# Optimization experiments

Measured on AMD Instinct MI355X. Metric: run time of the kernel, lower is better.

The kernel has to match this reference:

```python
import jax, jax.numpy as jnp
import numpy as np

B, N, D, K, H, L = 4, 20000, 64, 256, 4, 2
F = 4 * D
DH = D // H
SCALE = DH ** -0.5
EPS = 1e-5


def _layernorm(x, g, b):
    m = jnp.mean(x, axis=-1, keepdims=True)
    v = jnp.mean(jnp.square(x - m), axis=-1, keepdims=True)
    return (x - m) / jnp.sqrt(v + EPS) * g + b


def setup_inputs() -> dict:
    key = jax.random.key(0)
    ks = jax.random.split(key, 12)
    s = 0.02
    return {
        'expr': jax.random.normal(ks[0], (B, N), jnp.float32),
        'emb': jax.random.normal(ks[1], (N, D), jnp.float32),
        'Wq': jax.random.normal(ks[2], (L, D, D), jnp.float32) * s,
        'Wk': jax.random.normal(ks[3], (L, D, D), jnp.float32) * s,
        'Wv': jax.random.normal(ks[4], (L, D, D), jnp.float32) * s,
        'projK': jax.random.normal(ks[5], (L, N, K), jnp.float32) * s,
        'projV': jax.random.normal(ks[6], (L, N, K), jnp.float32) * s,
        'Wo': jax.random.normal(ks[7], (L, D, D), jnp.float32) * s,
        'bo': jnp.zeros((L, D), jnp.float32),
        'g1': jnp.ones((L, D), jnp.float32),
        'be1': jnp.zeros((L, D), jnp.float32),
        'W1': jax.random.normal(ks[8], (L, D, F), jnp.float32) * s,
        'bf1': jnp.zeros((L, F), jnp.float32),
        'W2': jax.random.normal(ks[9], (L, F, D), jnp.float32) * s,
        'bf2': jnp.zeros((L, D), jnp.float32),
        'g2': jnp.ones((L, D), jnp.float32),
        'be2': jnp.zeros((L, D), jnp.float32),
    }


def _forward(expr, emb, Wq, Wk, Wv, projK, projV, Wo, bo, g1, be1, W1, bf1, W2, bf2, g2, be2):
    # gene_ids = arange(N) for every batch row -> embedding lookup is just the table
    x = emb[None, :, :] * expr[:, :, None]  # [B, N, D]
    for i in range(L):
        b = x.shape[0]
        # Linformer self-attention
        q = jnp.einsum('bnd,de->bne', x, Wq[i])                 # [B, N, D]
        k_low = jnp.einsum('bnd,nk->bkd', x, projK[i])          # [B, K, D]
        v_low = jnp.einsum('bnd,nk->bkd', x, projV[i])          # [B, K, D]
        k = jnp.einsum('bkd,de->bke', k_low, Wk[i])             # [B, K, D]
        v = jnp.einsum('bkd,de->bke', v_low, Wv[i])             # [B, K, D]
        qh = q.reshape(b, N, H, DH).transpose(0, 2, 1, 3)       # [B, H, N, DH]
        kh = k.reshape(b, K, H, DH).transpose(0, 2, 1, 3)       # [B, H, K, DH]
        vh = v.reshape(b, K, H, DH).transpose(0, 2, 1, 3)       # [B, H, K, DH]
        dots = jnp.einsum('bhnd,bhkd->bhnk', qh, kh) * SCALE    # [B, H, N, K]
        attn = jax.nn.softmax(dots, axis=-1)
        o = jnp.einsum('bhnk,bhkd->bhnd', attn, vh)             # [B, H, N, DH]
        o = o.transpose(0, 2, 1, 3).reshape(b, N, D)
        o = jnp.einsum('bnd,de->bne', o, Wo[i]) + bo[i]
        x = _layernorm(o + x, g1[i], be1[i])
        # FFN (exact GELU, matching torch nn.GELU default)
        h = jax.nn.gelu(jnp.einsum('bnd,df->bnf', x, W1[i]) + bf1[i], approximate=False)
        f = jnp.einsum('bnf,fd->bnd', h, W2[i]) + bf2[i]
        x = _layernorm(f + x, g2[i], be2[i])
    return x


def reference(expr, emb, Wq, Wk, Wv, projK, projV, Wo, bo, g1, be1, W1, bf1, W2, bf2, g2, be2):
    return _forward(expr, emb, Wq, Wk, Wv, projK, projV, Wo, bo, g1, be1, W1, bf1, W2, bf2, g2, be2)
```

## Files before the change

### kernel.cpp

```cpp
#include <hip/hip_runtime.h>

using u16 = unsigned short;
typedef __bf16 bf16x8 __attribute__((ext_vector_type(8)));
typedef u16    u16x8  __attribute__((ext_vector_type(8)));
typedef u16    u16x4  __attribute__((ext_vector_type(4)));
typedef float  f32x4  __attribute__((ext_vector_type(4)));
typedef float  f32x16 __attribute__((ext_vector_type(16)));
typedef unsigned uint4v __attribute__((ext_vector_type(4)));

#define DEV static __device__ __forceinline__

constexpr int NB = 4;
constexpr int NN = 20000;
constexpr int DD = 64;
constexpr int KK = 256;
constexpr int ROWS = NB * NN;

DEV float b2f(u16 u) { union { unsigned i; float f; } c; c.i = ((unsigned)u) << 16; return c.f; }
DEV u16 f2b(float f) {
  union { float f; unsigned i; } c; c.f = f;
  unsigned i = c.i + 0x7FFFu + ((c.i >> 16) & 1u);
  return (u16)(i >> 16);
}
DEV bf16x8 ldb8(const u16* p) { return *reinterpret_cast<const bf16x8*>(p); }
DEV f32x16 mfma32(bf16x8 a, bf16x8 b, f32x16 c) { return __builtin_amdgcn_mfma_f32_32x32x16_bf16(a, b, c, 0, 0, 0); }

DEV unsigned cvtpk(float lo, float hi) {
  unsigned r;
  asm("v_cvt_pk_bf16_f32 %0, %1, %2" : "=v"(r) : "v"(lo), "v"(hi));
  return r;
}
DEV void swap32(unsigned& a, unsigned& b) {
  auto r = __builtin_amdgcn_permlane32_swap((int)a, (int)b, false, false);
  a = (unsigned)r[0]; b = (unsigned)r[1];
}

__global__ __launch_bounds__(256) void k_pre(
    const float* __restrict__ expr, const float* __restrict__ emb,
    const float* __restrict__ Wq, const float* __restrict__ Wo,
    const float* __restrict__ W1, const float* __restrict__ W2,
    const float* __restrict__ projK, const float* __restrict__ projV,
    u16* __restrict__ wb, u16* __restrict__ pKT, u16* __restrict__ pVT,
    u16* __restrict__ xb, u16* __restrict__ ones) {
  int bid = blockIdx.x;
  int t = threadIdx.x;
  if (bid < 2512) {
    int nt = bid % 157, q = bid / 157, kt = q & 3, z = q >> 2;
    int layer = z & 1, pv = z >> 1;
    const float* src = (pv ? projV : projK) + (size_t)layer * NN * KK;
    u16* dst = (pv ? pVT : pKT) + (size_t)layer * KK * NN;
    int k = kt * 64 + (t & 63);
    int n0 = nt * 128 + (t >> 6) * 32;
    if (n0 >= NN) return;
    float v[32];
#pragma unroll
    for (int i = 0; i < 32; ++i) v[i] = src[(size_t)(n0 + i) * KK + k];
    unsigned ov[16];
#pragma unroll
    for (int i2 = 0; i2 < 16; ++i2) ov[i2] = cvtpk(v[2 * i2], v[2 * i2 + 1]);
    u16* drow = dst + (size_t)k * NN + n0;
#pragma unroll
    for (int p = 0; p < 4; ++p) {
      uint4v o; o.x = ov[p * 4 + 0]; o.y = ov[p * 4 + 1]; o.z = ov[p * 4 + 2]; o.w = ov[p * 4 + 3];
      *reinterpret_cast<uint4v*>(&drow[p * 8]) = o;
    }
  } else if (bid < 5012) {
    int idx8 = ((bid - 2512) * 256 + t) * 8;
    int b = idx8 / (NN * DD);
    int rem = idx8 - b * (NN * DD);
    int n = rem >> 6, d = rem & 63;
    float4 e0 = *reinterpret_cast<const float4*>(&emb[(n << 6) + d]);
    float4 e1 = *reinterpret_cast<const float4*>(&emb[(n << 6) + d + 4]);
    float s = expr[b * NN + n];
    u16x8 o;
    o[0] = f2b(e0.x * s); o[1] = f2b(e0.y * s); o[2] = f2b(e0.z * s); o[3] = f2b(e0.w * s);
    o[4] = f2b(e1.x * s); o[5] = f2b(e1.y * s); o[6] = f2b(e1.z * s); o[7] = f2b(e1.w * s);
    *reinterpret_cast<u16x8*>(&xb[idx8]) = o;
  } else if (bid < 5076) {
    int b2 = bid - 5012;
    int bx = b2 & 7, m = (b2 >> 3) & 3, l = b2 >> 5;
    int slot = bx * 256 + t;
    u16x8 o;
    if (m <= 1) {
      if (slot >= 512) return;
      int s = slot >> 7, rem = slot & 127;
      int ct = rem >> 6, lane = rem & 63;
      int hi = lane >> 5, lo = lane & 31;
      const float* src = (m == 0 ? Wq : Wo) + l * 4096;
      u16* dst = wb + (m == 0 ? 0 : 8192) + l * 4096;
#pragma unroll
      for (int j = 0; j < 8; ++j) o[j] = f2b(src[(s * 16 + hi * 8 + j) * 64 + ct * 32 + lo]);
      *reinterpret_cast<u16x8*>(&dst[slot * 8]) = o;
    } else if (m == 2) {
      int ftile = slot >> 8, s = (slot >> 6) & 3, lane = slot & 63;
      int hi = lane >> 5, lo = lane & 31;
      const float* src = W1 + l * 16384;
      u16* dst = wb + 16384 + l * 16384;
#pragma unroll
      for (int j = 0; j < 8; ++j) o[j] = f2b(src[(s * 16 + hi * 8 + j) * 256 + ftile * 32 + lo]);
      *reinterpret_cast<u16x8*>(&dst[slot * 8]) = o;
    } else {
      int dtile = slot >> 10, s2 = (slot >> 6) & 15, lane = slot & 63;
      int hi = lane >> 5, lo = lane & 31;
      const float* src = W2 + l * 16384;
      u16* dst = wb + 49152 + l * 16384;
#pragma unroll
      for (int j = 0; j < 8; ++j) o[j] = f2b(src[(s2 * 16 + hi * 8 + j) * 64 + dtile * 32 + lo]);
      *reinterpret_cast<u16x8*>(&dst[slot * 8]) = o;
    }
  } else {
    ones[t] = 0x3F80;
  }
}

__global__ __launch_bounds__(256) void k_qxt(
    const u16* __restrict__ x, const u16* __restrict__ WB,
    u16* __restrict__ qb, u16* __restrict__ xT) {
  int bid = blockIdx.x;
  int t = threadIdx.x;
  if (bid < 625) {
    int w = t >> 6, lane = t & 63;
    int lo = lane & 31, hi = lane >> 5;
    int unit = bid * 4 + w;
    bf16x8 wf[4][2];
#pragma unroll
    for (int s = 0; s < 4; ++s)
#pragma unroll
      for (int ct = 0; ct < 2; ++ct) wf[s][ct] = ldb8(&WB[((s * 2 + ct) * 64 + lane) * 8]);
    f32x16 acc[2] = {};
    int r0 = unit * 32;
#pragma unroll
    for (int s = 0; s < 4; ++s) {
      bf16x8 a = ldb8(&x[(size_t)(r0 + lo) * 64 + s * 16 + hi * 8]);
      acc[0] = mfma32(a, wf[s][0], acc[0]);
      acc[1] = mfma32(a, wf[s][1], acc[1]);
    }
#pragma unroll
    for (int reg = 0; reg < 16; ++reg) {
      int row = r0 + (reg & 3) + 8 * (reg >> 2) + 4 * hi;
      qb[(size_t)row * 64 + lo] = f2b(acc[0][reg]);
      qb[(size_t)row * 64 + 32 + lo] = f2b(acc[1][reg]);
    }
  } else {
    int v = bid - 625;
    int nt = v % 157, b = v / 157;
    int d = t & 63;
    int n0 = nt * 128 + (t >> 6) * 32;
    if (n0 >= NN) return;
    const u16* xbp = x + (size_t)b * NN * 64;
    u16 vv[32];
#pragma unroll
    for (int i = 0; i < 32; ++i) vv[i] = xbp[(size_t)(n0 + i) * 64 + d];
    u16* dst = xT + (size_t)b * 64 * NN + (size_t)d * NN + n0;
#pragma unroll
    for (int p = 0; p < 4; ++p) {
      u16x8 o;
#pragma unroll
      for (int j = 0; j < 8; ++j) o[j] = vv[p * 8 + j];
      *reinterpret_cast<u16x8*>(&dst[p * 8]) = o;
    }
  }
}

__global__ __launch_bounds__(256) void k_proj(
    const u16* __restrict__ xT, const u16* __restrict__ pKT_l, const u16* __restrict__ pVT_l,
    float* __restrict__ part) {
  int c = blockIdx.x, b = blockIdx.y, proj = blockIdx.z;
  const u16* P = proj ? pVT_l : pKT_l;
  int t = threadIdx.x, w = t >> 6, lane = t & 63;
  int lo = lane & 31, hi = lane >> 5;
  int d0 = (w & 1) * 32;
  int kbase = (w >> 1) * 128;
  int n0 = c * 512;
  int rem = NN - n0;
  int steps = (rem < 512 ? rem : 512) >> 4;
  const u16* xr = xT + ((size_t)b * 64 + d0 + lo) * NN;
  f32x16 acc[4] = {};
  int s = 0;
  for (; s + 4 <= steps; s += 4) {
    bf16x8 a[4]; bf16x8 bv[4][4];
#pragma unroll
    for (int u = 0; u < 4; ++u) {
      int nb = n0 + (s + u) * 16 + hi * 8;
      a[u] = ldb8(&xr[nb]);
#pragma unroll
      for (int g = 0; g < 4; ++g) bv[u][g] = ldb8(&P[(size_t)(kbase + g * 32 + lo) * NN + nb]);
    }
#pragma unroll
    for (int u = 0; u < 4; ++u)
#pragma unroll
      for (int g = 0; g < 4; ++g) acc[g] = mfma32(a[u], bv[u][g], acc[g]);
  }
  for (; s < steps; ++s) {
    int nb = n0 + s * 16 + hi * 8;
    bf16x8 a = ldb8(&xr[nb]);
#pragma unroll
    for (int g = 0; g < 4; ++g) acc[g] = mfma32(a, ldb8(&P[(size_t)(kbase + g * 32 + lo) * NN + nb]), acc[g]);
  }
  float* dst = part + ((size_t)(proj * NB + b) * 40 + c) * (64 * 256);
#pragma unroll
  for (int g = 0; g < 4; ++g)
#pragma unroll
    for (int r = 0; r < 16; ++r) {
      int d = d0 + (r & 3) + 8 * (r >> 2) + 4 * hi;
      dst[d * 256 + kbase + g * 32 + lo] = acc[g][r];
    }
}

__global__ __launch_bounds__(256) void k_p2(
    const float* __restrict__ part, const float* __restrict__ Wk_l, const float* __restrict__ Wv_l,
    u16* __restrict__ kbuf, u16* __restrict__ vT) {
  int ks = blockIdx.x, b = blockIdx.y, proj = blockIdx.z;
  int k0 = ks * 8;
  const float* W = proj ? Wv_l : Wk_l;
  __shared__ float low[64][8];
  int t = threadIdx.x;
  const float* src = part + (size_t)(proj * NB + b) * 40 * (64 * 256);
#pragma unroll
  for (int i = 0; i < 2; ++i) {
    int idx = i * 256 + t;
    int e = idx >> 3, k = idx & 7;
    float s = 0.f;
    for (int cc = 0; cc < 40; ++cc) s += src[(size_t)cc * (64 * 256) + e * 256 + k0 + k];
    low[e][k] = s;
  }
  __syncthreads();
#pragma unroll
  for (int i = 0; i < 2; ++i) {
    int idx = i * 256 + t;
    int d = idx & 63, kk = idx >> 6;
    float a = 0.f;
#pragma unroll
    for (int e = 0; e < 64; ++e) a += low[e][kk] * W[e * 64 + d];
    if (proj == 0) {
      kbuf[((size_t)b * KK + k0 + kk) * 64 + d] = f2b(a * 0.3606737602222409f);
    } else {
      vT[((size_t)b * 64 + d) * KK + k0 + kk] = f2b(a);
    }
  }
}

__global__ __launch_bounds__(256) void k_attn(
    const u16* __restrict__ q, const u16* __restrict__ kbuf, const u16* __restrict__ vT,
    const u16* __restrict__ ones, u16* __restrict__ ao) {
  int t = threadIdx.x, h = t >> 6, lane = t & 63;
  int lo = lane & 31, hi = lane >> 5;
  int b = blockIdx.y;
  int n0 = blockIdx.x * 32;
  const u16* qb = q + (size_t)b * NN * 64;
  const u16* kb = kbuf + (size_t)b * KK * 64 + h * 16;
  const u16* vsrc = (lo < 16)
      ? vT + (size_t)b * 64 * KK + (size_t)(h * 16 + lo) * KK
      : ones;
  bf16x8 qf = ldb8(&qb[(size_t)(n0 + lo) * 64 + h * 16 + hi * 8]);
  f32x16 acc = {};
#pragma unroll
  for (int kt = 0; kt < 8; ++kt) {
    bf16x8 kf = ldb8(&kb[(size_t)(kt * 32 + lo) * 64 + hi * 8]);
    f32x16 z = {};
    f32x16 s = mfma32(kf, qf, z);
    float e[16];
#pragma unroll
    for (int r = 0; r < 16; ++r) e[r] = __builtin_amdgcn_exp2f(s[r]);
#pragma unroll
    for (int c = 0; c < 2; ++c) {
      unsigned Aw = cvtpk(e[c * 8 + 0], e[c * 8 + 1]);
      unsigned Bw = cvtpk(e[c * 8 + 2], e[c * 8 + 3]);
      unsigned Cw = cvtpk(e[c * 8 + 4], e[c * 8 + 5]);
      unsigned Dw = cvtpk(e[c * 8 + 6], e[c * 8 + 7]);
      swap32(Aw, Cw);
      swap32(Bw, Dw);
      uint4v pk; pk.x = Aw; pk.y = Bw; pk.z = Cw; pk.w = Dw;
      bf16x8 af = ldb8(&vsrc[kt * 32 + c * 16 + hi * 8]);
      acc = mfma32(af, __builtin_bit_cast(bf16x8, pk), acc);
    }
  }
  float inv = __builtin_amdgcn_rcpf(acc[8]);
  float o[8];
#pragma unroll
  for (int r = 0; r < 8; ++r) o[r] = acc[r] * inv;
  unsigned Aw = cvtpk(o[0], o[1]);
  unsigned Bw = cvtpk(o[2], o[3]);
  unsigned Cw = cvtpk(o[4], o[5]);
  unsigned Dw = cvtpk(o[6], o[7]);
  swap32(Aw, Cw);
  swap32(Bw, Dw);
  uint4v st; st.x = Aw; st.y = Bw; st.z = Cw; st.w = Dw;
  *reinterpret_cast<uint4v*>(&ao[(size_t)b * NN * 64 + (size_t)(n0 + lo) * 64 + h * 16 + hi * 8]) = st;
}

__global__ __launch_bounds__(256) void k_oln(
    const u16* __restrict__ A, const u16* __restrict__ WB,
    const float* __restrict__ bias, const u16* __restrict__ res,
    const float* __restrict__ g, const float* __restrict__ be, u16* __restrict__ out) {
  int t = threadIdx.x, w = t >> 6, lane = t & 63;
  int lo = lane & 31, hi = lane >> 5;
  int unit = blockIdx.x * 4 + w;
  bf16x8 wf[4][2];
#pragma unroll
  for (int s = 0; s < 4; ++s)
#pragma unroll
    for (int ct = 0; ct < 2; ++ct) wf[s][ct] = ldb8(&WB[((s * 2 + ct) * 64 + lane) * 8]);
  float bia[2], gg[2], bb[2];
#pragma unroll
  for (int ct = 0; ct < 2; ++ct) {
    bia[ct] = bias[ct * 32 + lo];
    gg[ct] = g[ct * 32 + lo];
    bb[ct] = be[ct * 32 + lo];
  }
  f32x16 acc[2] = {};
  int r0 = unit * 32;
#pragma unroll
  for (int s = 0; s < 4; ++s) {
    bf16x8 a = ldb8(&A[(size_t)(r0 + lo) * 64 + s * 16 + hi * 8]);
    acc[0] = mfma32(a, wf[s][0], acc[0]);
    acc[1] = mfma32(a, wf[s][1], acc[1]);
  }
#pragma unroll
  for (int reg = 0; reg < 16; ++reg) {
    int row = r0 + (reg & 3) + 8 * (reg >> 2) + 4 * hi;
    float a0 = acc[0][reg] + bia[0] + b2f(res[(size_t)row * 64 + lo]);
    float a1 = acc[1][reg] + bia[1] + b2f(res[(size_t)row * 64 + 32 + lo]);
    float su = a0 + a1, sq = a0 * a0 + a1 * a1;
#pragma unroll
    for (int m = 1; m <= 16; m <<= 1) { su += __shfl_xor(su, m); sq += __shfl_xor(sq, m); }
    float mean = su * (1.f / 64.f);
    float var = sq * (1.f / 64.f) - mean * mean;
    float rstd = rsqrtf(var + 1e-5f);
    out[(size_t)row * 64 + lo] = f2b((a0 - mean) * rstd * gg[0] + bb[0]);
    out[(size_t)row * 64 + 32 + lo] = f2b((a1 - mean) * rstd * gg[1] + bb[1]);
  }
}

__global__ __launch_bounds__(256) void k_ffn(
    const u16* __restrict__ A, const u16* __restrict__ W1T, const u16* __restrict__ W2T,
    const float* __restrict__ b1, const float* __restrict__ b2,
    const float* __restrict__ g, const float* __restrict__ be,
    u16* __restrict__ outb, float* __restrict__ outf) {
  int t = threadIdx.x, w = t >> 6, lane = t & 63;
  int lo = lane & 31, hi = lane >> 5;
  int unit = blockIdx.x * 4 + w;
  int r0 = unit * 32;
  bf16x8 xf[4];
#pragma unroll
  for (int s = 0; s < 4; ++s) xf[s] = ldb8(&A[(size_t)(r0 + lo) * 64 + s * 16 + hi * 8]);
  f32x16 oacc[2] = {};
#pragma unroll
  for (int ft = 0; ft < 8; ++ft) {
    f32x16 hacc = {};
#pragma unroll
    for (int s = 0; s < 4; ++s)
      hacc = mfma32(ldb8(&W1T[((ft * 4 + s) * 64 + lane) * 8]), xf[s], hacc);
    float4 bb[4];
#pragma unroll
    for (int g4 = 0; g4 < 4; ++g4)
      bb[g4] = *reinterpret_cast<const float4*>(&b1[ft * 32 + g4 * 8 + 4 * hi]);
    float e[16];
#pragma unroll
    for (int r = 0; r < 16; ++r) {
      float z = hacc[r] + bb[r >> 2][r & 3];
      e[r] = 0.5f * z * (1.f + erff(z * 0.7071067811865475f));
    }
#pragma unroll
    for (int c = 0; c < 2; ++c) {
      unsigned Aw = cvtpk(e[c * 8 + 0], e[c * 8 + 1]);
      unsigned Bw = cvtpk(e[c * 8 + 2], e[c * 8 + 3]);
      unsigned Cw = cvtpk(e[c * 8 + 4], e[c * 8 + 5]);
      unsigned Dw = cvtpk(e[c * 8 + 6], e[c * 8 + 7]);
      swap32(Aw, Cw);
      swap32(Bw, Dw);
      uint4v pk; pk.x = Aw; pk.y = Bw; pk.z = Cw; pk.w = Dw;
      bf16x8 pf = __builtin_bit_cast(bf16x8, pk);
#pragma unroll
      for (int dt = 0; dt < 2; ++dt)
        oacc[dt] = mfma32(ldb8(&W2T[((dt * 16 + ft * 2 + c) * 64 + lane) * 8]), pf, oacc[dt]);
    }
  }
  int n = r0 + lo;
  float su = 0.f, sq = 0.f;
#pragma unroll
  for (int dt = 0; dt < 2; ++dt) {
#pragma unroll
    for (int m4 = 0; m4 < 4; ++m4) {
      int d0 = dt * 32 + m4 * 8 + 4 * hi;
      u16x4 rv = *reinterpret_cast<const u16x4*>(&A[(size_t)n * 64 + d0]);
      float4 b2v = *reinterpret_cast<const float4*>(&b2[d0]);
#pragma unroll
      for (int j = 0; j < 4; ++j) {
        int r = m4 * 4 + j;
        float val = oacc[dt][r] + b2v[j] + b2f(rv[j]);
        oacc[dt][r] = val;
        su += val; sq += val * val;
      }
    }
  }
  su += __shfl_xor(su, 32);
  sq += __shfl_xor(sq, 32);
  float mean = su * (1.f / 64.f);
  float var = sq * (1.f / 64.f) - mean * mean;
  float rstd = rsqrtf(var + 1e-5f);
#pragma unroll
  for (int dt = 0; dt < 2; ++dt) {
#pragma unroll
    for (int m4 = 0; m4 < 4; ++m4) {
      int d0 = dt * 32 + m4 * 8 + 4 * hi;
      float4 gv = *reinterpret_cast<const float4*>(&g[d0]);
      float4 bv = *reinterpret_cast<const float4*>(&be[d0]);
      float q0 = (oacc[dt][m4 * 4 + 0] - mean) * rstd * gv.x + bv.x;
      float q1 = (oacc[dt][m4 * 4 + 1] - mean) * rstd * gv.y + bv.y;
      float q2 = (oacc[dt][m4 * 4 + 2] - mean) * rstd * gv.z + bv.z;
      float q3 = (oacc[dt][m4 * 4 + 3] - mean) * rstd * gv.w + bv.w;
      if (outb) {
        unsigned w0 = cvtpk(q0, q1), w1 = cvtpk(q2, q3);
        u16x4 st = __builtin_bit_cast(u16x4, make_uint2(w0, w1));
        *reinterpret_cast<u16x4*>(&outb[(size_t)n * 64 + d0]) = st;
      }
      if (outf) {
        *reinterpret_cast<float4*>(&outf[(size_t)n * 64 + d0]) = make_float4(q0, q1, q2, q3);
      }
    }
  }
}

extern "C" void kernel_launch(void* const* d_in, const int* in_sizes, int n_in,
                              void* d_out, int out_size, void* d_ws, size_t ws_size,
                              hipStream_t stream) {
  const float* expr = (const float*)d_in[0];
  const float* emb  = (const float*)d_in[1];
  const float* Wq   = (const float*)d_in[2];
  const float* Wk   = (const float*)d_in[3];
  const float* Wv   = (const float*)d_in[4];
  const float* projK = (const float*)d_in[5];
  const float* projV = (const float*)d_in[6];
  const float* Wo   = (const float*)d_in[7];
  const float* bo   = (const float*)d_in[8];
  const float* g1   = (const float*)d_in[9];
  const float* be1  = (const float*)d_in[10];
  const float* W1   = (const float*)d_in[11];
  const float* bf1  = (const float*)d_in[12];
  const float* W2   = (const float*)d_in[13];
  const float* bf2  = (const float*)d_in[14];
  const float* g2   = (const float*)d_in[15];
  const float* be2  = (const float*)d_in[16];
  float* out = (float*)d_out;
  char* ws = (char*)d_ws;

  u16* xb0 = (u16*)(ws + 0);
  u16* xb1 = (u16*)(ws + 10240000);
  u16* xb2 = (u16*)(ws + 20480000);
  u16* qb  = (u16*)(ws + 30720000);
  u16* aob = (u16*)(ws + 40960000);
  float* part = (float*)(ws + 51200000);
  u16* pKT = (u16*)(ws + 92160000);
  u16* pVT = (u16*)(ws + 112640000);
  u16* xTb = (u16*)(ws + 133120000);
  u16* kB  = (u16*)(ws + 143360000);
  u16* vTB = (u16*)(ws + 143491072);
  u16* wb  = (u16*)(ws + 143622144);
  u16* ones = (u16*)(ws + 143785984);

  k_pre<<<5077, 256, 0, stream>>>(expr, emb, Wq, Wo, W1, W2, projK, projV,
                                  wb, pKT, pVT, xb0, ones);

  const u16* xin = xb0;
  for (int l = 0; l < 2; ++l) {
    const u16* wbq = wb + l * 4096;
    const u16* wbo = wb + 8192 + l * 4096;
    const u16* wb1 = wb + 16384 + l * 16384;
    const u16* wb2 = wb + 49152 + l * 16384;
    k_qxt<<<1253, 256, 0, stream>>>(xin, wbq, qb, xTb);
    k_proj<<<dim3(40, NB, 2), 256, 0, stream>>>(xTb, pKT + (size_t)l * KK * NN, pVT + (size_t)l * KK * NN, part);
    k_p2<<<dim3(32, NB, 2), 256, 0, stream>>>(part, Wk + l * 4096, Wv + l * 4096, kB, vTB);
    k_attn<<<dim3(625, NB), 256, 0, stream>>>(qb, kB, vTB, ones, aob);
    k_oln<<<625, 256, 0, stream>>>(aob, wbo, bo + l * 64, xin, g1 + l * 64, be1 + l * 64, xb1);
    k_ffn<<<625, 256, 0, stream>>>(xb1, wb1, wb2, bf1 + l * 256, bf2 + l * 64,
                                   g2 + l * 64, be2 + l * 64,
                                   l == 0 ? xb2 : nullptr, l == 1 ? out : nullptr);
    xin = xb2;
  }
}
```

Before: 413.5 us.

## Tile projection and transposed-x buffers in 64-column blocks via LDS transposes

The transposed projK/projV and x^T buffers now use a tiled layout of 64-wide n tiles, so each tile is a contiguous block of K×64 or 64×64. The transpose kernels stage data through shared memory with swizzling or padding, which gives coalesced loads and stores in place of strided per-element gathers. k_proj indexes into the tiled layout so its per-lane loads stay inside contiguous tiles. This trades the extra LDS traffic and a barrier for much better global memory access in the preprocessing and transpose stages.

```diff
diff --git a/kernel.cpp b/kernel.cpp
--- a/kernel.cpp
+++ b/kernel.cpp
@@ -14,6 +14,7 @@
 constexpr int NN = 20000;
 constexpr int DD = 64;
 constexpr int KK = 256;
+constexpr int NT = 313;
 constexpr int ROWS = NB * NN;
 
 DEV float b2f(u16 u) { union { unsigned i; float f; } c; c.i = ((unsigned)u) << 16; return c.f; }
@@ -42,30 +43,46 @@
     const float* __restrict__ projK, const float* __restrict__ projV,
     u16* __restrict__ wb, u16* __restrict__ pKT, u16* __restrict__ pVT,
     u16* __restrict__ xb, u16* __restrict__ ones) {
+  __shared__ unsigned Lt[256][33];
   int bid = blockIdx.x;
   int t = threadIdx.x;
-  if (bid < 2512) {
-    int nt = bid % 157, q = bid / 157, kt = q & 3, z = q >> 2;
+  if (bid < 1252) {
+    int tile = bid % NT, z = bid / NT;
     int layer = z & 1, pv = z >> 1;
     const float* src = (pv ? projV : projK) + (size_t)layer * NN * KK;
-    u16* dst = (pv ? pVT : pKT) + (size_t)layer * KK * NN;
-    int k = kt * 64 + (t & 63);
-    int n0 = nt * 128 + (t >> 6) * 32;
-    if (n0 >= NN) return;
-    float v[32];
-#pragma unroll
-    for (int i = 0; i < 32; ++i) v[i] = src[(size_t)(n0 + i) * KK + k];
-    unsigned ov[16];
-#pragma unroll
-    for (int i2 = 0; i2 < 16; ++i2) ov[i2] = cvtpk(v[2 * i2], v[2 * i2 + 1]);
-    u16* drow = dst + (size_t)k * NN + n0;
-#pragma unroll
-    for (int p = 0; p < 4; ++p) {
-      uint4v o; o.x = ov[p * 4 + 0]; o.y = ov[p * 4 + 1]; o.z = ov[p * 4 + 2]; o.w = ov[p * 4 + 3];
-      *reinterpret_cast<uint4v*>(&drow[p * 8]) = o;
-    }
-  } else if (bid < 5012) {
-    int idx8 = ((bid - 2512) * 256 + t) * 8;
+    u16* dst = (pv ? pVT : pKT) + ((size_t)layer * NT + tile) * (256 * 64);
+    int w = t >> 6, l = t & 63;
+    int n0 = tile * 64;
+    float4 v[16];
+#pragma unroll
+    for (int i = 0; i < 16; ++i) {
+      int n = n0 + w * 16 + i;
+      v[i] = (n < NN) ? reinterpret_cast<const float4*>(src)[(size_t)n * 64 + l]
+                      : make_float4(0.f, 0.f, 0.f, 0.f);
+    }
+    int swz = ((l >> 1) & 7) << 2;
+#pragma unroll
+    for (int j = 0; j < 8; ++j) {
+      int npx = (w * 8 + j) ^ swz;
+#pragma unroll
+      for (int c = 0; c < 4; ++c) {
+        float a = (&v[2 * j].x)[c], b = (&v[2 * j + 1].x)[c];
+        Lt[4 * l + c][npx] = cvtpk(a, b);
+      }
+    }
+    __syncthreads();
+    int q = t & 7, kk = t >> 3;
+#pragma unroll
+    for (int p = 0; p < 8; ++p) {
+      int k = p * 32 + kk;
+      int base = (q * 4) ^ (((k >> 3) & 7) << 2);
+      uint4v o;
+      o.x = Lt[k][base + 0]; o.y = Lt[k][base + 1];
+      o.z = Lt[k][base + 2]; o.w = Lt[k][base + 3];
+      *reinterpret_cast<uint4v*>(&dst[(size_t)k * 64 + q * 8]) = o;
+    }
+  } else if (bid < 3752) {
+    int idx8 = ((bid - 1252) * 256 + t) * 8;
     int b = idx8 / (NN * DD);
     int rem = idx8 - b * (NN * DD);
     int n = rem >> 6, d = rem & 63;
@@ -76,8 +93,8 @@
     o[0] = f2b(e0.x * s); o[1] = f2b(e0.y * s); o[2] = f2b(e0.z * s); o[3] = f2b(e0.w * s);
     o[4] = f2b(e1.x * s); o[5] = f2b(e1.y * s); o[6] = f2b(e1.z * s); o[7] = f2b(e1.w * s);
     *reinterpret_cast<u16x8*>(&xb[idx8]) = o;
-  } else if (bid < 5076) {
-    int b2 = bid - 5012;
+  } else if (bid < 3816) {
+    int b2 = bid - 3752;
     int bx = b2 & 7, m = (b2 >> 3) & 3, l = b2 >> 5;
     int slot = bx * 256 + t;
     u16x8 o;
@@ -116,6 +133,7 @@
 __global__ __launch_bounds__(256) void k_qxt(
     const u16* __restrict__ x, const u16* __restrict__ WB,
     u16* __restrict__ qb, u16* __restrict__ xT) {
+  __shared__ u16 LX[64][67];
   int bid = blockIdx.x;
   int t = threadIdx.x;
   if (bid < 625) {
@@ -142,22 +160,29 @@
       qb[(size_t)row * 64 + 32 + lo] = f2b(acc[1][reg]);
     }
   } else {
-    int v = bid - 625;
-    int nt = v % 157, b = v / 157;
-    int d = t & 63;
-    int n0 = nt * 128 + (t >> 6) * 32;
-    if (n0 >= NN) return;
+    int v2 = bid - 625;
+    int tile = v2 % NT, b = v2 / NT;
     const u16* xbp = x + (size_t)b * NN * 64;
-    u16 vv[32];
-#pragma unroll
-    for (int i = 0; i < 32; ++i) vv[i] = xbp[(size_t)(n0 + i) * 64 + d];
-    u16* dst = xT + (size_t)b * 64 * NN + (size_t)d * NN + n0;
-#pragma unroll
-    for (int p = 0; p < 4; ++p) {
+    int n0 = tile * 64;
+    int q = t & 7, rr = t >> 3;
+    u16x8 h0 = {}, h1 = {};
+    int na = n0 + rr, nb2 = n0 + 32 + rr;
+    if (na < NN) h0 = *reinterpret_cast<const u16x8*>(&xbp[(size_t)na * 64 + q * 8]);
+    if (nb2 < NN) h1 = *reinterpret_cast<const u16x8*>(&xbp[(size_t)nb2 * 64 + q * 8]);
+#pragma unroll
+    for (int c = 0; c < 8; ++c) {
+      LX[q * 8 + c][rr] = h0[c];
+      LX[q * 8 + c][32 + rr] = h1[c];
+    }
+    __syncthreads();
+    u16* dstx = xT + ((size_t)b * NT + tile) * 4096;
+#pragma unroll
+    for (int p = 0; p < 2; ++p) {
+      int d = p * 32 + rr;
       u16x8 o;
 #pragma unroll
-      for (int j = 0; j < 8; ++j) o[j] = vv[p * 8 + j];
-      *reinterpret_cast<u16x8*>(&dst[p * 8]) = o;
+      for (int i = 0; i < 8; ++i) o[i] = LX[d][q * 8 + i];
+      *reinterpret_cast<u16x8*>(&dstx[(size_t)d * 64 + q * 8]) = o;
     }
   }
 }
@@ -167,6 +192,7 @@
     float* __restrict__ part) {
   int c = blockIdx.x, b = blockIdx.y, proj = blockIdx.z;
   const u16* P = proj ? pVT_l : pKT_l;
+  const u16* xtb = xT + (size_t)b * NT * 4096;
   int t = threadIdx.x, w = t >> 6, lane = t & 63;
   int lo = lane & 31, hi = lane >> 5;
   int d0 = (w & 1) * 32;
@@ -174,17 +200,20 @@
   int n0 = c * 512;
   int rem = NN - n0;
   int steps = (rem < 512 ? rem : 512) >> 4;
-  const u16* xr = xT + ((size_t)b * 64 + d0 + lo) * NN;
+  int arow = (d0 + lo) * 64;
   f32x16 acc[4] = {};
   int s = 0;
   for (; s + 4 <= steps; s += 4) {
+    int tile = (n0 + s * 16) >> 6;
+    const u16* xa = xtb + (size_t)tile * 4096;
+    const u16* Pa = P + (size_t)tile * 16384;
     bf16x8 a[4]; bf16x8 bv[4][4];
 #pragma unroll
     for (int u = 0; u < 4; ++u) {
-      int nb = n0 + (s + u) * 16 + hi * 8;
-      a[u] = ldb8(&xr[nb]);
-#pragma unroll
-      for (int g = 0; g < 4; ++g) bv[u][g] = ldb8(&P[(size_t)(kbase + g * 32 + lo) * NN + nb]);
+      int ni = u * 16 + hi * 8;
+      a[u] = ldb8(&xa[arow + ni]);
+#pragma unroll
+      for (int g = 0; g < 4; ++g) bv[u][g] = ldb8(&Pa[(kbase + g * 32 + lo) * 64 + ni]);
     }
 #pragma unroll
     for (int u = 0; u < 4; ++u)
@@ -192,10 +221,13 @@
       for (int g = 0; g < 4; ++g) acc[g] = mfma32(a[u], bv[u][g], acc[g]);
   }
   for (; s < steps; ++s) {
-    int nb = n0 + s * 16 + hi * 8;
-    bf16x8 a = ldb8(&xr[nb]);
-#pragma unroll
-    for (int g = 0; g < 4; ++g) acc[g] = mfma32(a, ldb8(&P[(size_t)(kbase + g * 32 + lo) * NN + nb]), acc[g]);
+    int nb = n0 + s * 16;
+    int tile = nb >> 6, ni = (nb & 63) + hi * 8;
+    const u16* xa = xtb + (size_t)tile * 4096;
+    const u16* Pa = P + (size_t)tile * 16384;
+    bf16x8 a = ldb8(&xa[arow + ni]);
+#pragma unroll
+    for (int g = 0; g < 4; ++g) acc[g] = mfma32(a, ldb8(&Pa[(kbase + g * 32 + lo) * 64 + ni]), acc[g]);
   }
   float* dst = part + ((size_t)(proj * NB + b) * 40 + c) * (64 * 256);
 #pragma unroll
@@ -451,25 +483,26 @@
   u16* qb  = (u16*)(ws + 30720000);
   u16* aob = (u16*)(ws + 40960000);
   float* part = (float*)(ws + 51200000);
-  u16* pKT = (u16*)(ws + 92160000);
-  u16* pVT = (u16*)(ws + 112640000);
-  u16* xTb = (u16*)(ws + 133120000);
-  u16* kB  = (u16*)(ws + 143360000);
-  u16* vTB = (u16*)(ws + 143491072);
-  u16* wb  = (u16*)(ws + 143622144);
-  u16* ones = (u16*)(ws + 143785984);
-
-  k_pre<<<5077, 256, 0, stream>>>(expr, emb, Wq, Wo, W1, W2, projK, projV,
+  u16* pKT = (u16*)(ws + 72171520);
+  u16* pVT = (u16*)(ws + 92684288);
+  u16* xTb = (u16*)(ws + 113197056);
+  u16* kB  = (u16*)(ws + 123453440);
+  u16* vTB = (u16*)(ws + 123584512);
+  u16* wb  = (u16*)(ws + 123715584);
+  u16* ones = (u16*)(ws + 123879424);
+
+  k_pre<<<3817, 256, 0, stream>>>(expr, emb, Wq, Wo, W1, W2, projK, projV,
                                   wb, pKT, pVT, xb0, ones);
 
+  const size_t PL = (size_t)NT * 256 * 64;
   const u16* xin = xb0;
   for (int l = 0; l < 2; ++l) {
     const u16* wbq = wb + l * 4096;
     const u16* wbo = wb + 8192 + l * 4096;
     const u16* wb1 = wb + 16384 + l * 16384;
     const u16* wb2 = wb + 49152 + l * 16384;
-    k_qxt<<<1253, 256, 0, stream>>>(xin, wbq, qb, xTb);
-    k_proj<<<dim3(40, NB, 2), 256, 0, stream>>>(xTb, pKT + (size_t)l * KK * NN, pVT + (size_t)l * KK * NN, part);
+    k_qxt<<<1877, 256, 0, stream>>>(xin, wbq, qb, xTb);
+    k_proj<<<dim3(40, NB, 2), 256, 0, stream>>>(xTb, pKT + (size_t)l * PL, pVT + (size_t)l * PL, part);
     k_p2<<<dim3(32, NB, 2), 256, 0, stream>>>(part, Wk + l * 4096, Wv + l * 4096, kB, vTB);
     k_attn<<<dim3(625, NB), 256, 0, stream>>>(qb, kB, vTB, ones, aob);
     k_oln<<<625, 256, 0, stream>>>(aob, wbo, bo + l * 64, xin, g1 + l * 64, be1 + l * 64, xb1);
```

Measured after the change: 422.6 us. 1.02x slower.
